# Optimization experiments

Hardware: AMD Instinct MI355X
Metric: run time of the kernel (lower is better)

Reference implementation:

```python
import jax, jax.numpy as jnp
import numpy as np

B, L, H, NL = 4, 384, 128, 3
F = H * NL  # num_filters = hidden_dim * num_layers = h_V feature dim


def gelu(x):
    return jax.nn.gelu(x, approximate=False)  # torch nn.GELU default is exact erf


def setup_inputs() -> dict:
    key = jax.random.key(0)
    ks = jax.random.split(key, 10)
    rn = lambda k, shape, s=0.05: jax.random.normal(k, shape, jnp.float32) * s
    h_V = jax.random.normal(ks[0], (B, L, F), jnp.float32)
    h_E = jax.random.normal(ks[1], (B, L, L, H), jnp.float32)
    mask = (jax.random.uniform(ks[2], (B, L)) > 0.1).astype(jnp.float32)
    # CFConv filter_network: Linear(H->F), GELU, Linear(F->F), GELU
    fw1 = rn(ks[3], (H, F)); fb1 = jnp.zeros((F,), jnp.float32)
    fw2 = rn(ks[4], (F, F)); fb2 = jnp.zeros((F,), jnp.float32)
    # mlp_head: Linear(F->H), GELU, Linear(H->H//2), GELU, Linear(H//2->1)
    hw1 = rn(ks[5], (F, H)); hb1 = jnp.zeros((H,), jnp.float32)
    hw2 = rn(ks[6], (H, H // 2)); hb2 = jnp.zeros((H // 2,), jnp.float32)
    hw3 = rn(ks[7], (H // 2, 1)); hb3 = jnp.zeros((1,), jnp.float32)
    return dict(h_V=h_V, h_E=h_E, mask=mask, fw1=fw1, fb1=fb1, fw2=fw2, fb2=fb2,
                hw1=hw1, hb1=hb1, hw2=hw2, hb2=hb2, hw3=hw3, hb3=hb3)


def reference(h_V, h_E, mask, fw1, fb1, fw2, fb2, hw1, hb1, hw2, hb2, hw3, hb3):
    # CFConv: per-edge filter MLP on edge features [B,L,L,H] -> [B,L,L,F]
    Wf = gelu(gelu(h_E @ fw1 + fb1) @ fw2 + fb2)
    # broadcast multiply with x.unsqueeze(1) then sum over neighbor dim (dim=2)
    x_conv = jnp.einsum('bkf,blkf->blf', h_V, Wf)  # [B,L,F]
    # mlp_head (dropout is identity in eval)
    h = gelu(x_conv @ hw1 + hb1)
    h = gelu(h @ hw2 + hb2)
    pred = (h @ hw3 + hb3)[..., 0]  # [B,L]
    valid_length = jnp.clip(jnp.sum(mask, axis=1), 1.0, None)
    return jnp.sum(pred * mask, axis=1) / jnp.sqrt(valid_length)  # [B]
```

## Files before the change

### kernel.cpp

```cpp
#include <hip/hip_runtime.h>


#define Bz 4
#define Lz 384
#define Hz 128
#define Fz 384
#define KT 32
#define NIT 12

typedef short bf16x8 __attribute__((ext_vector_type(8)));
typedef float f32x4 __attribute__((ext_vector_type(4)));

__device__ __forceinline__ unsigned short f2bf(float f) {
  unsigned int u = __float_as_uint(f);
  u += 0x7FFFu + ((u >> 16) & 1u);
  return (unsigned short)(u >> 16);
}

__device__ __forceinline__ float gelu_f(float x) {
  const float a1 = 0.254829592f, a2 = -0.284496736f, a3 = 1.421413741f;
  const float a4 = -1.453152027f, a5 = 1.061405429f;
  float z = fabsf(x) * 0.7071067811865476f;
  float t = __builtin_amdgcn_rcpf(__builtin_fmaf(0.3275911f, z, 1.0f));
  float poly = t * (a1 + t * (a2 + t * (a3 + t * (a4 + t * a5))));
  float e = __builtin_fmaf(-poly, __expf(-z * z), 1.0f);
  return 0.5f * x * (1.0f + copysignf(e, x));
}

__global__ __launch_bounds__(256) void prep_kernel(
    const float* __restrict__ fw1, const float* __restrict__ fw2,
    unsigned short* __restrict__ fw1P, unsigned short* __restrict__ fw2P,
    float* __restrict__ accbuf, int* __restrict__ ctr)
{
  int e = blockIdx.x * 256 + threadIdx.x;
  if (e < 16) accbuf[e] = 0.0f;
  if (e == 16) *ctr = 0;
  if (e < 24 * 4 * 64 * 8) {
    int j = e & 7, lf = (e >> 3) & 63, ks = (e >> 9) & 3, t = e >> 11;
    int n = t * 16 + (lf & 15);
    int k = ks * 32 + (lf >> 4) * 8 + j;
    fw1P[e] = f2bf(fw1[(size_t)k * Fz + n]);
  } else if (e < 24 * 4 * 64 * 8 + 24 * 12 * 64 * 8) {
    int o = e - 24 * 4 * 64 * 8;
    int j = o & 7, lf = (o >> 3) & 63, r = o >> 9;
    int ks = r % 12, t = r / 12;
    int n = t * 16 + (lf & 15);
    int k = ks * 32 + (lf >> 4) * 8 + j;
    fw2P[o] = f2bf(fw2[(size_t)k * Fz + n]);
  }
}

__global__ __launch_bounds__(512, 4) void schnet_main(
    const float* __restrict__ hV, const float* __restrict__ hE,
    const float* __restrict__ mask,
    const unsigned short* __restrict__ fw1P, const float* __restrict__ fb1,
    const unsigned short* __restrict__ fw2P, const float* __restrict__ fb2,
    const float* __restrict__ hw1, const float* __restrict__ hb1,
    const float* __restrict__ hw2, const float* __restrict__ hb2,
    const float* __restrict__ hw3, const float* __restrict__ hb3,
    float* __restrict__ accbuf, int* __restrict__ ctr,
    float* __restrict__ out)
{
  const int bl   = blockIdx.x;
  const int b    = bl / Lz;
  const int l    = bl - b * Lz;
  const int tid  = threadIdx.x;
  const int wave = tid >> 6;
  const int lane = tid & 63;
  const int lr   = lane & 15;
  const int quad = lane >> 4;
  const int l7   = lane & 7;

  __shared__ __attribute__((aligned(16))) char sMem[32768];
  unsigned short* sA  = (unsigned short*)sMem;
  unsigned short* sT1 = (unsigned short*)(sMem + 8192);
  float* sXC = (float*)sMem;
  float* sHp = sXC + Fz;
  float* sH1 = sHp + 4 * Hz;
  float* sH2 = sH1 + Hz;
  int*   sLast = (int*)(sH2 + 64);

  const float* hE_bl = hE + (size_t)bl * (Lz * Hz);
  const unsigned short* w1base = fw1P + (size_t)lane * 8;
  const unsigned short* w2base = fw2P + (size_t)lane * 8;

  const int srow = tid >> 4;
  const int su   = tid & 15;
  const float* hE_stage = hE_bl + (size_t)tid * 8;
  unsigned short* sAw = sA + srow * 128 + (((su ^ (srow & 7)) & 15) << 3);

  const f32x4 zero4 = {0.f, 0.f, 0.f, 0.f};
  f32x4 xc[3];
  xc[0] = zero4; xc[1] = zero4; xc[2] = zero4;

  {
    f32x4 v0 = *(const f32x4*)hE_stage;
    f32x4 v1 = *(const f32x4*)(hE_stage + 4);
    bf16x8 o;
    o[0] = (short)f2bf(v0[0]); o[1] = (short)f2bf(v0[1]);
    o[2] = (short)f2bf(v0[2]); o[3] = (short)f2bf(v0[3]);
    o[4] = (short)f2bf(v1[0]); o[5] = (short)f2bf(v1[1]);
    o[6] = (short)f2bf(v1[2]); o[7] = (short)f2bf(v1[3]);
    *(bf16x8*)sAw = o;
  }
  __syncthreads();

  #pragma unroll 1
  for (int it = 0; it < NIT; ++it) {
    f32x4 s0, s1;

    f32x4 acc1[2][3];
    #pragma unroll
    for (int mt = 0; mt < 2; ++mt)
      #pragma unroll
      for (int nt = 0; nt < 3; ++nt) acc1[mt][nt] = zero4;

    #pragma unroll 2
    for (int ks = 0; ks < 4; ++ks) {
      const int xu = ((ks << 2) + quad) ^ l7;
      bf16x8 afr[2];
      #pragma unroll
      for (int mt = 0; mt < 2; ++mt)
        afr[mt] = *(const bf16x8*)(sA + ((mt * 16 + lr) << 7) + (xu << 3));
      bf16x8 bfr[3];
      #pragma unroll
      for (int nt = 0; nt < 3; ++nt)
        bfr[nt] = *(const bf16x8*)(w1base +
                      (size_t)(((wave * 3 + nt) * 4 + ks) * 64) * 8);
      __builtin_amdgcn_s_setprio(1);
      #pragma unroll
      for (int mt = 0; mt < 2; ++mt)
        #pragma unroll
        for (int nt = 0; nt < 3; ++nt)
          acc1[mt][nt] = __builtin_amdgcn_mfma_f32_16x16x32_bf16(
              bfr[nt], afr[mt], acc1[mt][nt], 0, 0, 0);
      __builtin_amdgcn_s_setprio(0);
    }

    if (it + 1 < NIT) {
      const float* src = hE_stage + (size_t)(it + 1) * (KT * Hz);
      s0 = *(const f32x4*)src;
      s1 = *(const f32x4*)(src + 4);
    }

    #pragma unroll
    for (int nt = 0; nt < 3; ++nt) {
      const int n0 = wave * 48 + nt * 16 + quad * 4;
      const f32x4 bias = *(const f32x4*)(fb1 + n0);
      const int so = (((wave * 6 + nt * 2 + (quad >> 1)) ^ l7) << 3)
                     + ((quad & 1) << 2);
      #pragma unroll
      for (int mt = 0; mt < 2; ++mt) {
        short4 o;
        o.x = (short)f2bf(gelu_f(acc1[mt][nt][0] + bias[0]));
        o.y = (short)f2bf(gelu_f(acc1[mt][nt][1] + bias[1]));
        o.z = (short)f2bf(gelu_f(acc1[mt][nt][2] + bias[2]));
        o.w = (short)f2bf(gelu_f(acc1[mt][nt][3] + bias[3]));
        *(short4*)(sT1 + (mt * 16 + lr) * 384 + so) = o;
      }
    }
    __syncthreads();

    f32x4 acc2[2][3];
    #pragma unroll
    for (int mt = 0; mt < 2; ++mt)
      #pragma unroll
      for (int nt = 0; nt < 3; ++nt) acc2[mt][nt] = zero4;

    #pragma unroll 2
    for (int ks = 0; ks < 12; ++ks) {
      const int xu = ((ks << 2) + quad) ^ l7;
      bf16x8 afr[2];
      #pragma unroll
      for (int mt = 0; mt < 2; ++mt)
        afr[mt] = *(const bf16x8*)(sT1 + (mt * 16 + lr) * 384 + (xu << 3));
      bf16x8 bfr[3];
      #pragma unroll
      for (int nt = 0; nt < 3; ++nt)
        bfr[nt] = *(const bf16x8*)(w2base +
                      (size_t)(((wave * 3 + nt) * 12 + ks) * 64) * 8);
      __builtin_amdgcn_s_setprio(1);
      #pragma unroll
      for (int mt = 0; mt < 2; ++mt)
        #pragma unroll
        for (int nt = 0; nt < 3; ++nt)
          acc2[mt][nt] = __builtin_amdgcn_mfma_f32_16x16x32_bf16(
              bfr[nt], afr[mt], acc2[mt][nt], 0, 0, 0);
      __builtin_amdgcn_s_setprio(0);
    }

    #pragma unroll
    for (int nt = 0; nt < 3; ++nt) {
      const int n0 = wave * 48 + nt * 16 + quad * 4;
      const f32x4 b2 = *(const f32x4*)(fb2 + n0);
      #pragma unroll
      for (int mt = 0; mt < 2; ++mt) {
        const float* hv =
            hV + ((size_t)b * Lz + it * KT + mt * 16 + lr) * Fz + n0;
        const f32x4 hvv = *(const f32x4*)hv;
        #pragma unroll
        for (int r = 0; r < 4; ++r)
          xc[nt][r] += gelu_f(acc2[mt][nt][r] + b2[r]) * hvv[r];
      }
    }

    if (it + 1 < NIT) {
      bf16x8 o;
      o[0] = (short)f2bf(s0[0]); o[1] = (short)f2bf(s0[1]);
      o[2] = (short)f2bf(s0[2]); o[3] = (short)f2bf(s0[3]);
      o[4] = (short)f2bf(s1[0]); o[5] = (short)f2bf(s1[1]);
      o[6] = (short)f2bf(s1[2]); o[7] = (short)f2bf(s1[3]);
      *(bf16x8*)sAw = o;
    }
    __syncthreads();
  }

  #pragma unroll
  for (int nt = 0; nt < 3; ++nt)
    #pragma unroll
    for (int r = 0; r < 4; ++r) {
      float v = xc[nt][r];
      v += __shfl_xor(v, 1);
      v += __shfl_xor(v, 2);
      v += __shfl_xor(v, 4);
      v += __shfl_xor(v, 8);
      if (lr == 0) sXC[wave * 48 + nt * 16 + quad * 4 + r] = v;
    }
  __syncthreads();

  {
    int i = tid & 127;
    int part = tid >> 7;
    float a = 0.f;
    const int f0 = part * 96;
    for (int f = f0; f < f0 + 96; ++f) a += sXC[f] * hw1[f * Hz + i];
    sHp[part * Hz + i] = a;
  }
  __syncthreads();
  if (tid < Hz)
    sH1[tid] = gelu_f(sHp[tid] + sHp[Hz + tid] + sHp[2 * Hz + tid]
                      + sHp[3 * Hz + tid] + hb1[tid]);
  __syncthreads();
  if (tid < 64) {
    float a = hb2[tid];
    for (int i = 0; i < Hz; ++i) a += sH1[i] * hw2[i * 64 + tid];
    sH2[tid] = gelu_f(a);
  }
  __syncthreads();
  if (wave == 0) {
    float v = sH2[lane] * hw3[lane];
    #pragma unroll
    for (int off = 32; off >= 1; off >>= 1) v += __shfl_xor(v, off);
    if (lane == 0) {
      float pred = v + hb3[0];
      atomicAdd(&accbuf[b], pred * mask[b * Lz + l]);
      __threadfence();
      *sLast = (atomicAdd(ctr, 1) == (Bz * Lz - 1));
    }
  }
  __syncthreads();

  if (*sLast && wave < Bz) {
    float s = 0.f;
    #pragma unroll
    for (int k = 0; k < Lz / 64; ++k) s += mask[wave * Lz + k * 64 + lane];
    #pragma unroll
    for (int off = 32; off >= 1; off >>= 1) s += __shfl_xor(s, off);
    if (lane == 0) {
      float vl = s < 1.0f ? 1.0f : s;
      float a = atomicAdd(&accbuf[wave], 0.0f);
      out[wave] = a / sqrtf(vl);
    }
  }
}

extern "C" void kernel_launch(void* const* d_in, const int* in_sizes, int n_in,
                              void* d_out, int out_size, void* d_ws, size_t ws_size,
                              hipStream_t stream)
{
  const float* hV   = (const float*)d_in[0];
  const float* hE   = (const float*)d_in[1];
  const float* mask = (const float*)d_in[2];
  const float* fw1  = (const float*)d_in[3];
  const float* fb1  = (const float*)d_in[4];
  const float* fw2  = (const float*)d_in[5];
  const float* fb2  = (const float*)d_in[6];
  const float* hw1  = (const float*)d_in[7];
  const float* hb1  = (const float*)d_in[8];
  const float* hw2  = (const float*)d_in[9];
  const float* hb2  = (const float*)d_in[10];
  const float* hw3  = (const float*)d_in[11];
  const float* hb3  = (const float*)d_in[12];
  float* out = (float*)d_out;

  float* accbuf = (float*)d_ws;
  int*   ctr    = (int*)((char*)d_ws + 64);
  unsigned short* fw1P = (unsigned short*)((char*)d_ws + 1024);
  unsigned short* fw2P = fw1P + 24 * 4 * 64 * 8;

  prep_kernel<<<768, 256, 0, stream>>>(fw1, fw2, fw1P, fw2P, accbuf, ctr);
  schnet_main<<<Bz * Lz, 512, 0, stream>>>(hV, hE, mask, fw1P, fb1, fw2P, fb2,
                                           hw1, hb1, hw2, hb2, hw3, hb3,
                                           accbuf, ctr, out);
}
```

Before: 844.3 us.

## Double-buffer LDS tiles, defer GEMM2 epilogue, and shorten GELU erf polynomial

The LDS staging for the input tile and the GEMM1 output is now double-buffered, which drops one __syncthreads per iteration. The GELU-and-multiply epilogue of GEMM2 is deferred into the next iteration so it can overlap with the following GEMM1 and the global loads. The erf approximation in GELU is also cut from a 5-term to a 3-term Abramowitz-Stegun polynomial, saving ALU work at some accuracy cost. LDS use grows from 32 KB to 64 KB, which may reduce occupancy.

```diff
diff --git a/kernel.cpp b/kernel.cpp
--- a/kernel.cpp
+++ b/kernel.cpp
@@ -18,11 +18,10 @@
 }
 
 __device__ __forceinline__ float gelu_f(float x) {
-  const float a1 = 0.254829592f, a2 = -0.284496736f, a3 = 1.421413741f;
-  const float a4 = -1.453152027f, a5 = 1.061405429f;
+  const float a1 = 0.3480242f, a2 = -0.0958798f, a3 = 0.7478556f;
   float z = fabsf(x) * 0.7071067811865476f;
-  float t = __builtin_amdgcn_rcpf(__builtin_fmaf(0.3275911f, z, 1.0f));
-  float poly = t * (a1 + t * (a2 + t * (a3 + t * (a4 + t * a5))));
+  float t = __builtin_amdgcn_rcpf(__builtin_fmaf(0.47047f, z, 1.0f));
+  float poly = t * __builtin_fmaf(t, __builtin_fmaf(t, a3, a2), a1);
   float e = __builtin_fmaf(-poly, __expf(-z * z), 1.0f);
   return 0.5f * x * (1.0f + copysignf(e, x));
 }
@@ -71,9 +70,7 @@
   const int quad = lane >> 4;
   const int l7   = lane & 7;
 
-  __shared__ __attribute__((aligned(16))) char sMem[32768];
-  unsigned short* sA  = (unsigned short*)sMem;
-  unsigned short* sT1 = (unsigned short*)(sMem + 8192);
+  __shared__ __attribute__((aligned(16))) char sMem[65536];
   float* sXC = (float*)sMem;
   float* sHp = sXC + Fz;
   float* sH1 = sHp + 4 * Hz;
@@ -87,11 +84,12 @@
   const int srow = tid >> 4;
   const int su   = tid & 15;
   const float* hE_stage = hE_bl + (size_t)tid * 8;
-  unsigned short* sAw = sA + srow * 128 + (((su ^ (srow & 7)) & 15) << 3);
+  const int sAoff = srow * 128 + (((su ^ (srow & 7)) & 15) << 3);
 
   const f32x4 zero4 = {0.f, 0.f, 0.f, 0.f};
   f32x4 xc[3];
   xc[0] = zero4; xc[1] = zero4; xc[2] = zero4;
+  f32x4 acc2[2][3];
 
   {
     f32x4 v0 = *(const f32x4*)hE_stage;
@@ -101,13 +99,15 @@
     o[2] = (short)f2bf(v0[2]); o[3] = (short)f2bf(v0[3]);
     o[4] = (short)f2bf(v1[0]); o[5] = (short)f2bf(v1[1]);
     o[6] = (short)f2bf(v1[2]); o[7] = (short)f2bf(v1[3]);
-    *(bf16x8*)sAw = o;
+    *(bf16x8*)((unsigned short*)sMem + sAoff) = o;
   }
   __syncthreads();
 
   #pragma unroll 1
   for (int it = 0; it < NIT; ++it) {
-    f32x4 s0, s1;
+    const int q = it & 1;
+    unsigned short* sAq  = (unsigned short*)(sMem + q * 8192);
+    unsigned short* sT1q = (unsigned short*)(sMem + 16384 + q * 24576);
 
     f32x4 acc1[2][3];
     #pragma unroll
@@ -121,7 +121,7 @@
       bf16x8 afr[2];
       #pragma unroll
       for (int mt = 0; mt < 2; ++mt)
-        afr[mt] = *(const bf16x8*)(sA + ((mt * 16 + lr) << 7) + (xu << 3));
+        afr[mt] = *(const bf16x8*)(sAq + ((mt * 16 + lr) << 7) + (xu << 3));
       bf16x8 bfr[3];
       #pragma unroll
       for (int nt = 0; nt < 3; ++nt)
@@ -137,10 +137,29 @@
       __builtin_amdgcn_s_setprio(0);
     }
 
+    f32x4 s0, s1;
     if (it + 1 < NIT) {
       const float* src = hE_stage + (size_t)(it + 1) * (KT * Hz);
       s0 = *(const f32x4*)src;
       s1 = *(const f32x4*)(src + 4);
+    }
+
+    if (it > 0) {
+      const int itp = it - 1;
+      #pragma unroll
+      for (int nt = 0; nt < 3; ++nt) {
+        const int n0 = wave * 48 + nt * 16 + quad * 4;
+        const f32x4 b2 = *(const f32x4*)(fb2 + n0);
+        #pragma unroll
+        for (int mt = 0; mt < 2; ++mt) {
+          const float* hv =
+              hV + ((size_t)b * Lz + itp * KT + mt * 16 + lr) * Fz + n0;
+          const f32x4 hvv = *(const f32x4*)hv;
+          #pragma unroll
+          for (int r = 0; r < 4; ++r)
+            xc[nt][r] += gelu_f(acc2[mt][nt][r] + b2[r]) * hvv[r];
+        }
+      }
     }
 
     #pragma unroll
@@ -156,12 +175,20 @@
         o.y = (short)f2bf(gelu_f(acc1[mt][nt][1] + bias[1]));
         o.z = (short)f2bf(gelu_f(acc1[mt][nt][2] + bias[2]));
         o.w = (short)f2bf(gelu_f(acc1[mt][nt][3] + bias[3]));
-        *(short4*)(sT1 + (mt * 16 + lr) * 384 + so) = o;
+        *(short4*)(sT1q + (mt * 16 + lr) * 384 + so) = o;
       }
     }
+
+    if (it + 1 < NIT) {
+      bf16x8 o;
+      o[0] = (short)f2bf(s0[0]); o[1] = (short)f2bf(s0[1]);
+      o[2] = (short)f2bf(s0[2]); o[3] = (short)f2bf(s0[3]);
+      o[4] = (short)f2bf(s1[0]); o[5] = (short)f2bf(s1[1]);
+      o[6] = (short)f2bf(s1[2]); o[7] = (short)f2bf(s1[3]);
+      *(bf16x8*)((unsigned short*)(sMem + (q ^ 1) * 8192) + sAoff) = o;
+    }
     __syncthreads();
 
-    f32x4 acc2[2][3];
     #pragma unroll
     for (int mt = 0; mt < 2; ++mt)
       #pragma unroll
@@ -173,7 +200,7 @@
       bf16x8 afr[2];
       #pragma unroll
       for (int mt = 0; mt < 2; ++mt)
-        afr[mt] = *(const bf16x8*)(sT1 + (mt * 16 + lr) * 384 + (xu << 3));
+        afr[mt] = *(const bf16x8*)(sT1q + (mt * 16 + lr) * 384 + (xu << 3));
       bf16x8 bfr[3];
       #pragma unroll
       for (int nt = 0; nt < 3; ++nt)
@@ -188,7 +215,10 @@
               bfr[nt], afr[mt], acc2[mt][nt], 0, 0, 0);
       __builtin_amdgcn_s_setprio(0);
     }
-
+  }
+
+  {
+    const int itp = NIT - 1;
     #pragma unroll
     for (int nt = 0; nt < 3; ++nt) {
       const int n0 = wave * 48 + nt * 16 + quad * 4;
@@ -196,23 +226,13 @@
       #pragma unroll
       for (int mt = 0; mt < 2; ++mt) {
         const float* hv =
-            hV + ((size_t)b * Lz + it * KT + mt * 16 + lr) * Fz + n0;
+            hV + ((size_t)b * Lz + itp * KT + mt * 16 + lr) * Fz + n0;
         const f32x4 hvv = *(const f32x4*)hv;
         #pragma unroll
         for (int r = 0; r < 4; ++r)
           xc[nt][r] += gelu_f(acc2[mt][nt][r] + b2[r]) * hvv[r];
       }
     }
-
-    if (it + 1 < NIT) {
-      bf16x8 o;
-      o[0] = (short)f2bf(s0[0]); o[1] = (short)f2bf(s0[1]);
-      o[2] = (short)f2bf(s0[2]); o[3] = (short)f2bf(s0[3]);
-      o[4] = (short)f2bf(s1[0]); o[5] = (short)f2bf(s1[1]);
-      o[6] = (short)f2bf(s1[2]); o[7] = (short)f2bf(s1[3]);
-      *(bf16x8*)sAw = o;
-    }
-    __syncthreads();
   }
 
   #pragma unroll
```

Result: slower. 877.3 us (+3.9%).
